# Performance work log

Measured on AMD Instinct MI355X. Metric: run time of the kernel, lower is better.

The kernel has to match this reference:

```python
import jax, jax.numpy as jnp
import numpy as np

D_MODEL = 1024
D_INNER = 2048        # expand=2
D_STATE = 128
NHEADS = 16           # d_inner / headdim
HEADDIM = 128
D_CONV = 4
D_XBC = D_INNER + 2 * D_STATE          # 2304 (ngroups=1)
D_IN_PROJ = 2 * D_INNER + 2 * D_STATE + NHEADS  # 4368
BATCH, SEQLEN = 2, 2048
EPS = 1e-5


def setup_inputs() -> dict:
    key = jax.random.key(0)
    ks = jax.random.split(key, 8)
    f = jnp.float32
    return {
        "x": jax.random.normal(ks[0], (BATCH, SEQLEN, D_MODEL), f),
        "ln_w": jnp.ones((D_MODEL,), f),
        "ln_b": jnp.zeros((D_MODEL,), f),
        "W_in": jax.random.normal(ks[1], (D_MODEL, D_IN_PROJ), f) * 0.02,
        "conv_w": jax.random.normal(ks[2], (D_XBC, D_CONV), f) * 0.2,
        "conv_b": jnp.zeros((D_XBC,), f),
        "dt_bias": jax.random.uniform(ks[3], (NHEADS,), f, -4.0, -2.0),
        "A_log": jnp.log(jax.random.uniform(ks[4], (NHEADS,), f, 1.0, 16.0)),
        "D": jnp.ones((NHEADS,), f),
        "rms_w": jnp.ones((D_INNER,), f),
        "W_out": jax.random.normal(ks[5], (D_INNER, D_MODEL), f) * 0.02,
    }


def _mamba_wrap(x, ln_w, ln_b, W_in, conv_w, conv_b, dt_bias, A_log, D, rms_w, W_out):
    B, L = x.shape[0], x.shape[1]
    # LayerNorm (pre-norm)
    mu = jnp.mean(x, -1, keepdims=True)
    var = jnp.mean(jnp.square(x - mu), -1, keepdims=True)
    xn = (x - mu) * jax.lax.rsqrt(var + EPS) * ln_w + ln_b
    # input projection -> z, xBC, dt
    zxbcdt = xn @ W_in                               # (B,L,4368)
    z = zxbcdt[..., :D_INNER]                        # (B,L,2048)
    xBC = zxbcdt[..., D_INNER:D_INNER + D_XBC]       # (B,L,2304)
    dt = jax.nn.softplus(zxbcdt[..., -NHEADS:] + dt_bias)  # (B,L,16)
    # causal depthwise conv1d (kernel 4), then SiLU
    xp = jnp.pad(xBC, ((0, 0), (D_CONV - 1, 0), (0, 0)))
    taps = jnp.stack([xp[:, k:k + L, :] for k in range(D_CONV)], axis=-1)  # (B,L,C,K)
    xBC = jax.nn.silu(jnp.einsum('blck,ck->blc', taps, conv_w) + conv_b)
    # split into SSM inputs
    xh = xBC[..., :D_INNER].reshape(B, L, NHEADS, HEADDIM)   # (B,L,H,P)
    Bm = xBC[..., D_INNER:D_INNER + D_STATE]                  # (B,L,N) ngroups=1
    Cm = xBC[..., D_INNER + D_STATE:]                         # (B,L,N)
    A = -jnp.exp(A_log)                                       # (H,)
    dA = jnp.exp(dt * A)                                      # (B,L,H)

    def step(state, inp):
        xt, dtt, dAt, Bt, Ct = inp  # (B,H,P),(B,H),(B,H),(B,N),(B,N)
        state = state * dAt[..., None, None] + (dtt[..., None] * xt)[..., None] * Bt[:, None, None, :]
        y = jnp.einsum('bhpn,bn->bhp', state, Ct)
        return state, y

    init = jnp.zeros((B, NHEADS, HEADDIM, D_STATE), x.dtype)
    xs = (xh.transpose(1, 0, 2, 3), dt.transpose(1, 0, 2), dA.transpose(1, 0, 2),
          Bm.transpose(1, 0, 2), Cm.transpose(1, 0, 2))
    _, ys = jax.lax.scan(step, init, xs)                      # (L,B,H,P)
    y = ys.transpose(1, 0, 2, 3) + D[None, None, :, None] * xh  # skip term
    y = y.reshape(B, L, D_INNER)
    # gated RMSNorm: rmsnorm(y * silu(z)) * weight
    y = y * jax.nn.silu(z)
    y = y * jax.lax.rsqrt(jnp.mean(y * y, -1, keepdims=True) + EPS) * rms_w
    # output projection + residual
    return x + y @ W_out


def reference(x, ln_w, ln_b, W_in, conv_w, conv_b, dt_bias, A_log, D, rms_w, W_out):
    return _mamba_wrap(x, ln_w, ln_b, W_in, conv_w, conv_b, dt_bias, A_log, D, rms_w, W_out)
```

## Files before the change

kernel.cpp:

```cpp
#include <hip/hip_runtime.h>

typedef unsigned short ushort_t;
typedef __attribute__((ext_vector_type(8))) unsigned short ushort8;
typedef __attribute__((ext_vector_type(4))) unsigned short ushortv4;
typedef __attribute__((ext_vector_type(8))) __bf16 bf16x8;
typedef __attribute__((ext_vector_type(4))) float f32x4;

#define BATCH   2
#define SEQLEN  2048
#define BL      4096
#define DMODEL  1024
#define DINNER  2048
#define DSTATE  128
#define NHEADS  16
#define DXBC    2304
#define DPROJ   4368
#define NPAD    4480
#define EPSF    1e-5f
#define QCH     128
#define NCH     16
#define BH      32

#define SWZ(row, colbyte) ((colbyte) ^ (((row) & 7) << 4))

#define GLDS(gp, lp) __builtin_amdgcn_global_load_lds( \
    (const __attribute__((address_space(1))) void*)(gp), \
    (__attribute__((address_space(3))) void*)(lp), 16, 0, 0)

__device__ __forceinline__ float bf2f(ushort_t h) {
    unsigned int u = ((unsigned int)h) << 16;
    float f; __builtin_memcpy(&f, &u, 4); return f;
}
__device__ __forceinline__ ushort_t f2bf(float f) {
    unsigned int u; __builtin_memcpy(&u, &f, 4);
    unsigned int r = u + 0x7fffu + ((u >> 16) & 1u);
    return (ushort_t)(r >> 16);
}
__device__ __forceinline__ float siluf(float x) { return x / (1.f + expf(-x)); }
__device__ __forceinline__ float softplusf(float x) { return (x > 20.f) ? x : log1pf(expf(x)); }

__global__ __launch_bounds__(256) void ln_kernel(const float* __restrict__ x,
        const float* __restrict__ w, const float* __restrict__ b, ushort_t* __restrict__ xn) {
    int r = blockIdx.x, t = threadIdx.x;
    const float* xr = x + (size_t)r * DMODEL;
    float4 v = *(const float4*)&xr[t * 4];
    float s  = v.x + v.y + v.z + v.w;
    float sq = v.x*v.x + v.y*v.y + v.z*v.z + v.w*v.w;
    __shared__ float red[8];
    #pragma unroll
    for (int m = 32; m >= 1; m >>= 1) { s += __shfl_xor(s, m, 64); sq += __shfl_xor(sq, m, 64); }
    int wv = t >> 6;
    if ((t & 63) == 0) { red[wv] = s; red[4 + wv] = sq; }
    __syncthreads();
    s  = red[0] + red[1] + red[2] + red[3];
    sq = red[4] + red[5] + red[6] + red[7];
    float mu  = s * (1.f / DMODEL);
    float var = sq * (1.f / DMODEL) - mu * mu;
    float inv = rsqrtf(var + EPSF);
    float4 wv4 = *(const float4*)&w[t * 4];
    float4 bv4 = *(const float4*)&b[t * 4];
    ushortv4 o;
    o[0] = f2bf((v.x - mu) * inv * wv4.x + bv4.x);
    o[1] = f2bf((v.y - mu) * inv * wv4.y + bv4.y);
    o[2] = f2bf((v.z - mu) * inv * wv4.z + bv4.z);
    o[3] = f2bf((v.w - mu) * inv * wv4.w + bv4.w);
    *(ushortv4*)&xn[(size_t)r * DMODEL + t * 4] = o;
}

__global__ __launch_bounds__(256) void transpose_cast(const float* __restrict__ W,
        ushort_t* __restrict__ WT, int K, int N) {
    __shared__ float tile[32][33];
    int n0 = blockIdx.x * 32, k0 = blockIdx.y * 32;
    int tx = threadIdx.x & 31, ty = threadIdx.x >> 5;
    #pragma unroll
    for (int i = 0; i < 32; i += 8) {
        int n = n0 + tx;
        tile[ty + i][tx] = (n < N) ? W[(size_t)(k0 + ty + i) * N + n] : 0.f;
    }
    __syncthreads();
    #pragma unroll
    for (int i = 0; i < 32; i += 8) {
        WT[(size_t)(n0 + ty + i) * K + k0 + tx] = f2bf(tile[tx][ty + i]);
    }
}

__global__ __launch_bounds__(256) void convw_tr(const float* __restrict__ w,
        float* __restrict__ wt) {
    int c = blockIdx.x * 256 + threadIdx.x;
    if (c < DXBC) {
        float4 v = *(const float4*)&w[c * 4];
        wt[0 * DXBC + c] = v.x;
        wt[1 * DXBC + c] = v.y;
        wt[2 * DXBC + c] = v.z;
        wt[3 * DXBC + c] = v.w;
    }
}

template <bool OUTBF>
__global__ __launch_bounds__(256) void gemm_bt(const ushort_t* __restrict__ A,
        const ushort_t* __restrict__ BT, void* __restrict__ Cv,
        const float* __restrict__ resid, int K, int ldc, int nbx) {
    const int tid = threadIdx.x;
    const int nwg = gridDim.x;
    const int cpx = nwg >> 3;
    const int lid = (blockIdx.x & 7) * cpx + (blockIdx.x >> 3);
    const int m0 = (lid / nbx) * 128, n0 = (lid % nbx) * 128;
    __shared__ ushort_t As[3][128 * 32];
    __shared__ ushort_t Bs[3][128 * 32];
    const int lane = tid & 63, wave = tid >> 6;
    const int wrow = wave * 32;
    const int srow = lane >> 2;
    const int selm = ((lane & 3) ^ (srow & 3)) * 8;
    const ushort_t* ag0 = A  + (size_t)(m0 + wrow + srow) * K + selm;
    const ushort_t* ag1 = ag0 + (size_t)16 * K;
    const ushort_t* bg0 = BT + (size_t)(n0 + wrow + srow) * K + selm;
    const ushort_t* bg1 = bg0 + (size_t)16 * K;
    const int wm = (wave >> 1) * 64, wn = (wave & 1) * 64;
    const int fr = lane & 15, ko = (lane >> 4) * 8;
    f32x4 acc[4][4];
    #pragma unroll
    for (int i = 0; i < 4; i++)
        #pragma unroll
        for (int j = 0; j < 4; j++) acc[i][j] = (f32x4){0.f, 0.f, 0.f, 0.f};
    const int nt = K >> 5;
    #pragma unroll
    for (int t = 0; t < 3; t++) {
        const size_t kof = (size_t)t * 32;
        GLDS(ag0 + kof, &As[t][wrow * 32]);
        GLDS(ag1 + kof, &As[t][(wrow + 16) * 32]);
        GLDS(bg0 + kof, &Bs[t][wrow * 32]);
        GLDS(bg1 + kof, &Bs[t][(wrow + 16) * 32]);
    }
    asm volatile("s_waitcnt vmcnt(8)" ::: "memory");
    __builtin_amdgcn_s_barrier();
    int cur = 0;
    for (int t = 0; t < nt; ++t) {
        if (t + 2 < nt) {
            int nb = cur + 2; if (nb >= 3) nb -= 3;
            const size_t kof = (size_t)(t + 2) * 32;
            GLDS(ag0 + kof, &As[nb][wrow * 32]);
            GLDS(ag1 + kof, &As[nb][(wrow + 16) * 32]);
            GLDS(bg0 + kof, &Bs[nb][wrow * 32]);
            GLDS(bg1 + kof, &Bs[nb][(wrow + 16) * 32]);
        }
        bf16x8 af[4], bfr[4];
        #pragma unroll
        for (int i = 0; i < 4; i++) {
            int row = wm + i * 16 + fr;
            af[i] = *(const bf16x8*)((const char*)&As[cur][0] + row * 64
                                     + ((ko * 2) ^ ((row & 3) << 4)));
        }
        #pragma unroll
        for (int j = 0; j < 4; j++) {
            int row = wn + j * 16 + fr;
            bfr[j] = *(const bf16x8*)((const char*)&Bs[cur][0] + row * 64
                                      + ((ko * 2) ^ ((row & 3) << 4)));
        }
        #pragma unroll
        for (int i = 0; i < 4; i++)
            #pragma unroll
            for (int j = 0; j < 4; j++)
                acc[i][j] = __builtin_amdgcn_mfma_f32_16x16x32_bf16(af[i], bfr[j], acc[i][j], 0, 0, 0);
        if (t + 2 < nt) asm volatile("s_waitcnt vmcnt(4)" ::: "memory");
        else            asm volatile("s_waitcnt vmcnt(0)" ::: "memory");
        __builtin_amdgcn_s_barrier();
        cur = (cur == 2) ? 0 : cur + 1;
    }
    const int r0 = (lane >> 4) * 4;
    #pragma unroll
    for (int i = 0; i < 4; i++)
        #pragma unroll
        for (int j = 0; j < 4; j++)
            #pragma unroll
            for (int r = 0; r < 4; r++) {
                int m = m0 + wm + i * 16 + r0 + r;
                int n = n0 + wn + j * 16 + fr;
                float v = acc[i][j][r];
                if (OUTBF) {
                    ((ushort_t*)Cv)[(size_t)m * ldc + n] = f2bf(v);
                } else {
                    if (resid) v += resid[(size_t)m * ldc + n];
                    ((float*)Cv)[(size_t)m * ldc + n] = v;
                }
            }
}

__global__ __launch_bounds__(256) void conv_kernel(const ushort_t* __restrict__ zxb,
        const float* __restrict__ wtr, const float* __restrict__ conv_b,
        const float* __restrict__ dt_bias, const float* __restrict__ A_log,
        ushort_t* __restrict__ xcv, ushort_t* __restrict__ Bcg, ushort_t* __restrict__ Ccg,
        float* __restrict__ dtv, float* __restrict__ dta) {
    int bid = blockIdx.x;
    int l = bid & (SEQLEN - 1);
    int tid = threadIdx.x;
    const ushort_t* rowp = zxb + (size_t)bid * NPAD;
    #pragma unroll 1
    for (int u = tid; u < DXBC / 8; u += 256) {
        int c0 = u * 8;
        float acc[8];
        {
            float4 b0 = *(const float4*)&conv_b[c0];
            float4 b1 = *(const float4*)&conv_b[c0 + 4];
            acc[0] = b0.x; acc[1] = b0.y; acc[2] = b0.z; acc[3] = b0.w;
            acc[4] = b1.x; acc[5] = b1.y; acc[6] = b1.z; acc[7] = b1.w;
        }
        #pragma unroll
        for (int k = 0; k < 4; k++) {
            int ll = l - 3 + k;
            if (ll >= 0) {
                ushort8 xv = *(const ushort8*)&rowp[(ptrdiff_t)(k - 3) * NPAD + DINNER + c0];
                float4 w0 = *(const float4*)&wtr[k * DXBC + c0];
                float4 w1 = *(const float4*)&wtr[k * DXBC + c0 + 4];
                acc[0] += bf2f((ushort_t)xv[0]) * w0.x;
                acc[1] += bf2f((ushort_t)xv[1]) * w0.y;
                acc[2] += bf2f((ushort_t)xv[2]) * w0.z;
                acc[3] += bf2f((ushort_t)xv[3]) * w0.w;
                acc[4] += bf2f((ushort_t)xv[4]) * w1.x;
                acc[5] += bf2f((ushort_t)xv[5]) * w1.y;
                acc[6] += bf2f((ushort_t)xv[6]) * w1.z;
                acc[7] += bf2f((ushort_t)xv[7]) * w1.w;
            }
        }
        ushort8 o;
        #pragma unroll
        for (int e = 0; e < 8; e++) o[e] = f2bf(siluf(acc[e]));
        if (c0 < DINNER)                *(ushort8*)&xcv[(size_t)bid * DINNER + c0] = o;
        else if (c0 < DINNER + DSTATE)  *(ushort8*)&Bcg[(size_t)bid * DSTATE + (c0 - DINNER)] = o;
        else                            *(ushort8*)&Ccg[(size_t)bid * DSTATE + (c0 - DINNER - DSTATE)] = o;
    }
    if (tid < NHEADS) {
        float raw = bf2f(rowp[DINNER + DXBC + tid]) + dt_bias[tid];
        float dt = softplusf(raw);
        float A = -expf(A_log[tid]);
        dtv[(size_t)bid * NHEADS + tid] = dt;
        dta[(size_t)bid * NHEADS + tid] = dt * A;
    }
}

__global__ __launch_bounds__(128) void cumsum_kernel(const float* __restrict__ dta,
        const float* __restrict__ dtv, float* __restrict__ cabuf, float* __restrict__ expca,
        float* __restrict__ wbuf, float* __restrict__ dtbuf, float* __restrict__ dtot) {
    const int c = blockIdx.x, h = blockIdx.y, b = blockIdx.z;
    const int bh = b * NHEADS + h;
    const int j = threadIdx.x;
    const size_t row = (size_t)b * SEQLEN + c * QCH + j;
    float v  = dta[row * NHEADS + h];
    float dt = dtv[row * NHEADS + h];
    float pv = v;
    #pragma unroll
    for (int off = 1; off < 64; off <<= 1) {
        float u = __shfl_up(pv, off, 64);
        if ((j & 63) >= off) pv += u;
    }
    __shared__ float wsum[2];
    if ((j & 63) == 63) wsum[j >> 6] = pv;
    __syncthreads();
    float tot = wsum[0] + wsum[1];
    if (j >= 64) pv += wsum[0];
    const size_t idx = ((size_t)bh * NCH + c) * QCH + j;
    cabuf[idx] = pv;
    expca[idx] = expf(pv);
    wbuf[idx]  = expf(tot - pv) * dt;
    dtbuf[idx] = dt;
    if (j == 0) dtot[bh * NCH + c] = expf(tot);
}

__global__ __launch_bounds__(256) void chunkstate_kernel(const ushort_t* __restrict__ xcv,
        const ushort_t* __restrict__ Bcg, const float* __restrict__ wbuf,
        ushort_t* __restrict__ states) {
    const int c = blockIdx.x, h = blockIdx.y, b = blockIdx.z;
    const int bh = b * NHEADS + h;
    const int tid = threadIdx.x;
    __shared__ ushort_t Xt[128 * 128];
    __shared__ ushort_t Bt[128 * 128];
    __shared__ float wsh[QCH];
    if (tid < QCH) wsh[tid] = wbuf[((size_t)bh * NCH + c) * QCH + tid];
    __syncthreads();
    const size_t row0 = (size_t)b * SEQLEN + c * QCH;
    {
        const int f = tid & 127;
        const int jh = (tid >> 7) * 64;
        const ushort_t* xsrc = xcv + (row0 + jh) * DINNER + h * 128 + f;
        const ushort_t* bsrc = Bcg + (row0 + jh) * DSTATE + f;
        char* xrow = (char*)Xt + f * 256;
        char* brow = (char*)Bt + f * 256;
        #pragma unroll 2
        for (int e8 = 0; e8 < 8; e8++) {
            ushort8 tx, tb;
            #pragma unroll
            for (int e = 0; e < 8; e++) {
                int j = e8 * 8 + e;
                tx[e] = xsrc[(size_t)j * DINNER];
                tb[e] = f2bf(bf2f(bsrc[(size_t)j * DSTATE]) * wsh[jh + j]);
            }
            int cb = (jh + e8 * 8) * 2;
            *(ushort8*)(xrow + SWZ(f, cb)) = tx;
            *(ushort8*)(brow + SWZ(f, cb)) = tb;
        }
    }
    __syncthreads();
    const int lane = tid & 63, wave = tid >> 6;
    const int wp = (wave >> 1) * 64, wn = (wave & 1) * 64;
    const int fr = lane & 15, ko = (lane >> 4) * 8;
    f32x4 acc[4][4];
    #pragma unroll
    for (int i = 0; i < 4; i++)
        #pragma unroll
        for (int j = 0; j < 4; j++) acc[i][j] = (f32x4){0.f, 0.f, 0.f, 0.f};
    for (int k0 = 0; k0 < 128; k0 += 32) {
        bf16x8 af[4], bfr[4];
        #pragma unroll
        for (int i = 0; i < 4; i++) {
            int rp = wp + i * 16 + fr;
            af[i] = *(const bf16x8*)((const char*)Xt + rp * 256 + SWZ(rp, (k0 + ko) * 2));
        }
        #pragma unroll
        for (int j = 0; j < 4; j++) {
            int rn = wn + j * 16 + fr;
            bfr[j] = *(const bf16x8*)((const char*)Bt + rn * 256 + SWZ(rn, (k0 + ko) * 2));
        }
        #pragma unroll
        for (int i = 0; i < 4; i++)
            #pragma unroll
            for (int j = 0; j < 4; j++)
                acc[i][j] = __builtin_amdgcn_mfma_f32_16x16x32_bf16(af[i], bfr[j], acc[i][j], 0, 0, 0);
    }
    const int r0 = (lane >> 4) * 4;
    ushort_t* outp = states + ((size_t)bh * NCH + c) * 16384;
    #pragma unroll
    for (int i = 0; i < 4; i++)
        #pragma unroll
        for (int j = 0; j < 4; j++)
            #pragma unroll
            for (int r = 0; r < 4; r++)
                outp[(wp + i * 16 + r0 + r) * 128 + wn + j * 16 + fr] = f2bf(acc[i][j][r]);
}

__global__ __launch_bounds__(256) void statescan_kernel(ushort_t* __restrict__ states,
        const float* __restrict__ dtot) {
    const int pseg = blockIdx.x, bh = blockIdx.y;
    const int tid = threadIdx.x;
    const int p = pseg * 8 + (tid >> 5);
    const int n4 = (tid & 31) * 4;
    ushort_t* base = states + (size_t)bh * NCH * 16384 + p * 128 + n4;
    const float* dtp = dtot + bh * NCH;
    float r0 = 0.f, r1 = 0.f, r2 = 0.f, r3 = 0.f;
    #pragma unroll 1
    for (int c = 0; c < NCH; c++) {
        ushortv4* ptr = (ushortv4*)(base + (size_t)c * 16384);
        ushortv4 cs = *ptr;
        ushortv4 o;
        o[0] = f2bf(r0); o[1] = f2bf(r1); o[2] = f2bf(r2); o[3] = f2bf(r3);
        *ptr = o;
        float d = dtp[c];
        r0 = r0 * d + bf2f(cs[0]);
        r1 = r1 * d + bf2f(cs[1]);
        r2 = r2 * d + bf2f(cs[2]);
        r3 = r3 * d + bf2f(cs[3]);
    }
}

__global__ __launch_bounds__(256) void chunkout_kernel(const ushort_t* __restrict__ xcv,
        const ushort_t* __restrict__ Bcg, const ushort_t* __restrict__ Ccg,
        const ushort_t* __restrict__ states, const float* __restrict__ cabuf,
        const float* __restrict__ expca, const float* __restrict__ dtbuf,
        const float* __restrict__ Dvec, ushort_t* __restrict__ yv) {
    const int c = blockIdx.x, h = blockIdx.y, b = blockIdx.z;
    const int bh = b * NHEADS + h;
    const int tid = threadIdx.x;
    __shared__ ushort_t R1[128 * 128];
    __shared__ ushort_t R2[128 * 128];
    __shared__ float cash[QCH], dtsh[QCH], exsh[QCH];
    const size_t aidx = ((size_t)bh * NCH + c) * QCH;
    if (tid < QCH) {
        cash[tid] = cabuf[aidx + tid];
        dtsh[tid] = dtbuf[aidx + tid];
        exsh[tid] = expca[aidx + tid];
    }
    const size_t row0 = (size_t)b * SEQLEN + c * QCH;
    {
        const ushort_t* sp = states + ((size_t)bh * NCH + c) * 16384;
        #pragma unroll
        for (int it = 0; it < 8; it++) {
            int g = tid + it * 256;
            int r = g >> 4, n8 = (g & 15) * 8;
            ushort8 vc = *(const ushort8*)&Ccg[(row0 + r) * DSTATE + n8];
            ushort8 vs = *(const ushort8*)&sp[r * 128 + n8];
            int cb = n8 * 2;
            *(ushort8*)((char*)R2 + r * 256 + SWZ(r, cb)) = vc;
            *(ushort8*)((char*)R1 + r * 256 + SWZ(r, cb)) = vs;
        }
    }
    __syncthreads();
    const int lane = tid & 63, wave = tid >> 6;
    const int fr = lane & 15, ko = (lane >> 4) * 8, r0 = (lane >> 4) * 4;
    const int wty = (wave >> 1) * 64, wpy = (wave & 1) * 64;
    f32x4 y_[4][4];
    #pragma unroll
    for (int i = 0; i < 4; i++)
        #pragma unroll
        for (int j = 0; j < 4; j++) y_[i][j] = (f32x4){0.f, 0.f, 0.f, 0.f};
    for (int k0 = 0; k0 < 128; k0 += 32) {
        bf16x8 af[4], bfr[4];
        #pragma unroll
        for (int i = 0; i < 4; i++) {
            int rt = wty + i * 16 + fr;
            af[i] = *(const bf16x8*)((const char*)R2 + rt * 256 + SWZ(rt, (k0 + ko) * 2));
        }
        #pragma unroll
        for (int j = 0; j < 4; j++) {
            int rp = wpy + j * 16 + fr;
            bfr[j] = *(const bf16x8*)((const char*)R1 + rp * 256 + SWZ(rp, (k0 + ko) * 2));
        }
        #pragma unroll
        for (int i = 0; i < 4; i++)
            #pragma unroll
            for (int j = 0; j < 4; j++)
                y_[i][j] = __builtin_amdgcn_mfma_f32_16x16x32_bf16(af[i], bfr[j], y_[i][j], 0, 0, 0);
    }
    #pragma unroll
    for (int i = 0; i < 4; i++)
        #pragma unroll
        for (int r = 0; r < 4; r++) {
            float sc = exsh[wty + i * 16 + r0 + r];
            #pragma unroll
            for (int j = 0; j < 4; j++) y_[i][j][r] *= sc;
        }
    __syncthreads();
    #pragma unroll
    for (int it = 0; it < 8; it++) {
        int g = tid + it * 256;
        int r = g >> 4, n8 = (g & 15) * 8;
        ushort8 vb = *(const ushort8*)&Bcg[(row0 + r) * DSTATE + n8];
        *(ushort8*)((char*)R1 + r * 256 + SWZ(r, n8 * 2)) = vb;
    }
    __syncthreads();
    const int wj = (wave >> 1) * 64, wt = (wave & 1) * 64;
    f32x4 g_[4][4];
    #pragma unroll
    for (int i = 0; i < 4; i++)
        #pragma unroll
        for (int t = 0; t < 4; t++) g_[i][t] = (f32x4){0.f, 0.f, 0.f, 0.f};
    if (!(wj == 64 && wt == 0)) {
        for (int k0 = 0; k0 < 128; k0 += 32) {
            bf16x8 af[4], bfr[4];
            #pragma unroll
            for (int i = 0; i < 4; i++) {
                int rj = wj + i * 16 + fr;
                af[i] = *(const bf16x8*)((const char*)R1 + rj * 256 + SWZ(rj, (k0 + ko) * 2));
            }
            #pragma unroll
            for (int t = 0; t < 4; t++) {
                int rt = wt + t * 16 + fr;
                bfr[t] = *(const bf16x8*)((const char*)R2 + rt * 256 + SWZ(rt, (k0 + ko) * 2));
            }
            #pragma unroll
            for (int i = 0; i < 4; i++)
                #pragma unroll
                for (int t = 0; t < 4; t++)
                    g_[i][t] = __builtin_amdgcn_mfma_f32_16x16x32_bf16(af[i], bfr[t], g_[i][t], 0, 0, 0);
        }
    }
    __syncthreads();
    {
        const float Dh = Dvec[h];
        #pragma unroll
        for (int i = 0; i < 4; i++) {
            #pragma unroll
            for (int t = 0; t < 4; t++) {
                int tt = wt + t * 16 + fr;
                int jj0 = wj + i * 16 + r0;
                ushortv4 pk;
                #pragma unroll
                for (int r = 0; r < 4; r++) {
                    int jj = jj0 + r;
                    float val = 0.f;
                    if (jj <= tt) {
                        val = g_[i][t][r] * expf(cash[tt] - cash[jj]) * dtsh[jj];
                        if (jj == tt) val += Dh;
                    }
                    pk[r] = f2bf(val);
                }
                *(ushortv4*)((char*)R1 + tt * 256 + SWZ(tt, jj0 * 2)) = pk;
            }
        }
        const int f = tid & 127;
        const int jh = (tid >> 7) * 64;
        const ushort_t* xsrc = xcv + (row0 + jh) * DINNER + h * 128 + f;
        char* xrow = (char*)R2 + f * 256;
        #pragma unroll 2
        for (int e8 = 0; e8 < 8; e8++) {
            ushort8 tx;
            #pragma unroll
            for (int e = 0; e < 8; e++) tx[e] = xsrc[(size_t)(e8 * 8 + e) * DINNER];
            int cb = (jh + e8 * 8) * 2;
            *(ushort8*)(xrow + SWZ(f, cb)) = tx;
        }
    }
    __syncthreads();
    const int kmax = wty + 64;
    for (int k0 = 0; k0 < kmax; k0 += 32) {
        bf16x8 af[4], bfr[4];
        #pragma unroll
        for (int i = 0; i < 4; i++) {
            int rt = wty + i * 16 + fr;
            af[i] = *(const bf16x8*)((const char*)R1 + rt * 256 + SWZ(rt, (k0 + ko) * 2));
        }
        #pragma unroll
        for (int j = 0; j < 4; j++) {
            int rp = wpy + j * 16 + fr;
            bfr[j] = *(const bf16x8*)((const char*)R2 + rp * 256 + SWZ(rp, (k0 + ko) * 2));
        }
        #pragma unroll
        for (int i = 0; i < 4; i++)
            #pragma unroll
            for (int j = 0; j < 4; j++)
                y_[i][j] = __builtin_amdgcn_mfma_f32_16x16x32_bf16(af[i], bfr[j], y_[i][j], 0, 0, 0);
    }
    #pragma unroll
    for (int i = 0; i < 4; i++)
        #pragma unroll
        for (int j = 0; j < 4; j++)
            #pragma unroll
            for (int r = 0; r < 4; r++) {
                int t = wty + i * 16 + r0 + r;
                int p = wpy + j * 16 + fr;
                yv[(row0 + t) * DINNER + h * 128 + p] = f2bf(y_[i][j][r]);
            }
}

__global__ __launch_bounds__(256) void gate_rms(const ushort_t* __restrict__ yv,
        const ushort_t* __restrict__ zxb, const float* __restrict__ rms_w,
        ushort_t* __restrict__ ynorm) {
    int r = blockIdx.x, t = threadIdx.x;
    const ushort_t* yr = yv + (size_t)r * DINNER;
    const ushort_t* zr = zxb + (size_t)r * NPAD;
    ushort8 y8 = *(const ushort8*)&yr[t * 8];
    ushort8 z8 = *(const ushort8*)&zr[t * 8];
    float g[8];
    #pragma unroll
    for (int j = 0; j < 8; j++)
        g[j] = bf2f((ushort_t)y8[j]) * siluf(bf2f((ushort_t)z8[j]));
    float sq = 0.f;
    #pragma unroll
    for (int j = 0; j < 8; j++) sq += g[j] * g[j];
    __shared__ float red[4];
    #pragma unroll
    for (int m = 32; m >= 1; m >>= 1) sq += __shfl_xor(sq, m, 64);
    int wv = t >> 6;
    if ((t & 63) == 0) red[wv] = sq;
    __syncthreads();
    sq = red[0] + red[1] + red[2] + red[3];
    float scale = rsqrtf(sq * (1.f / DINNER) + EPSF);
    float4 w0 = *(const float4*)&rms_w[t * 8];
    float4 w1 = *(const float4*)&rms_w[t * 8 + 4];
    ushort8 o;
    o[0] = f2bf(g[0] * scale * w0.x);
    o[1] = f2bf(g[1] * scale * w0.y);
    o[2] = f2bf(g[2] * scale * w0.z);
    o[3] = f2bf(g[3] * scale * w0.w);
    o[4] = f2bf(g[4] * scale * w1.x);
    o[5] = f2bf(g[5] * scale * w1.y);
    o[6] = f2bf(g[6] * scale * w1.z);
    o[7] = f2bf(g[7] * scale * w1.w);
    *(ushort8*)&ynorm[(size_t)r * DINNER + t * 8] = o;
}

extern "C" void kernel_launch(void* const* d_in, const int* in_sizes, int n_in,
                              void* d_out, int out_size, void* d_ws, size_t ws_size,
                              hipStream_t stream) {
    (void)in_sizes; (void)n_in; (void)out_size; (void)ws_size;
    const float* x       = (const float*)d_in[0];
    const float* ln_w    = (const float*)d_in[1];
    const float* ln_b    = (const float*)d_in[2];
    const float* W_in    = (const float*)d_in[3];
    const float* conv_w  = (const float*)d_in[4];
    const float* conv_b  = (const float*)d_in[5];
    const float* dt_bias = (const float*)d_in[6];
    const float* A_log   = (const float*)d_in[7];
    const float* Dvec    = (const float*)d_in[8];
    const float* rms_w   = (const float*)d_in[9];
    const float* W_out   = (const float*)d_in[10];
    float* out = (float*)d_out;

    char* ws = (char*)d_ws;
    size_t off = 0;
    auto alloc = [&](size_t bytes) -> void* {
        void* p = ws + off;
        off += (bytes + 255) & ~(size_t)255;
        return p;
    };
    ushort_t* xn    = (ushort_t*)alloc((size_t)BL * DMODEL * 2);
    ushort_t* WinT  = (ushort_t*)alloc((size_t)NPAD * DMODEL * 2);
    ushort_t* zxb   = (ushort_t*)alloc((size_t)BL * NPAD * 2);
    ushort_t* xcv   = (ushort_t*)alloc((size_t)BL * DINNER * 2);
    ushort_t* Bcg   = (ushort_t*)alloc((size_t)BL * DSTATE * 2);
    ushort_t* Ccg   = (ushort_t*)alloc((size_t)BL * DSTATE * 2);
    float*    dtv   = (float*)   alloc((size_t)BL * NHEADS * 4);
    float*    dta   = (float*)   alloc((size_t)BL * NHEADS * 4);
    ushort_t* yv    = (ushort_t*)alloc((size_t)BL * DINNER * 2);
    ushort_t* ynorm = (ushort_t*)alloc((size_t)BL * DINNER * 2);
    ushort_t* WoutT = (ushort_t*)alloc((size_t)DMODEL * DINNER * 2);
    float*    wtr   = (float*)   alloc((size_t)4 * DXBC * 4);
    float*    cabuf = (float*)   alloc((size_t)BH * NCH * QCH * 4);
    float*    expcb = (float*)   alloc((size_t)BH * NCH * QCH * 4);
    float*    wbuf  = (float*)   alloc((size_t)BH * NCH * QCH * 4);
    float*    dtbuf = (float*)   alloc((size_t)BH * NCH * QCH * 4);
    float*    dtot  = (float*)   alloc((size_t)BH * NCH * 4);
    ushort_t* states= (ushort_t*)alloc((size_t)BH * NCH * 16384 * 2);

    ln_kernel<<<BL, 256, 0, stream>>>(x, ln_w, ln_b, xn);
    transpose_cast<<<dim3(NPAD / 32, DMODEL / 32), 256, 0, stream>>>(W_in, WinT, DMODEL, DPROJ);
    transpose_cast<<<dim3(DMODEL / 32, DINNER / 32), 256, 0, stream>>>(W_out, WoutT, DINNER, DMODEL);
    convw_tr<<<(DXBC + 255) / 256, 256, 0, stream>>>(conv_w, wtr);
    gemm_bt<true><<<(NPAD / 128) * (BL / 128), 256, 0, stream>>>(xn, WinT, zxb, nullptr, DMODEL, NPAD, NPAD / 128);
    conv_kernel<<<BL, 256, 0, stream>>>(zxb, wtr, conv_b, dt_bias, A_log, xcv, Bcg, Ccg, dtv, dta);
    cumsum_kernel<<<dim3(NCH, NHEADS, BATCH), 128, 0, stream>>>(dta, dtv, cabuf, expcb, wbuf, dtbuf, dtot);
    chunkstate_kernel<<<dim3(NCH, NHEADS, BATCH), 256, 0, stream>>>(xcv, Bcg, wbuf, states);
    statescan_kernel<<<dim3(16, BH), 256, 0, stream>>>(states, dtot);
    chunkout_kernel<<<dim3(NCH, NHEADS, BATCH), 256, 0, stream>>>(xcv, Bcg, Ccg, states, cabuf, expcb, dtbuf, Dvec, yv);
    gate_rms<<<BL, 256, 0, stream>>>(yv, zxb, rms_w, ynorm);
    gemm_bt<false><<<(DMODEL / 128) * (BL / 128), 256, 0, stream>>>(ynorm, WoutT, out, x, DINNER, DMODEL, DMODEL / 128);
}
```

Baseline: 208.3 us.

## Add 256x256-tile double-buffered GEMM for input projection

Introduces a new 512-thread GEMM kernel with 256x256 output tiles and 64-wide K steps, double-buffered through LDS with direct global-to-LDS loads, and uses it for the input projection. The projection width is padded to 4608 so it divides evenly into 256-column tiles. The larger tiles raise arithmetic intensity and cut redundant operand loads, but they use a lot of LDS and registers, which lowers occupancy. The grid also shrinks to 288 workgroups, which may balance poorly across the compute units. The padding adds extra wasted columns of compute.

```diff
diff --git a/kernel.cpp b/kernel.cpp
--- a/kernel.cpp
+++ b/kernel.cpp
@@ -15,7 +15,7 @@
 #define NHEADS  16
 #define DXBC    2304
 #define DPROJ   4368
-#define NPAD    4480
+#define NPAD    4608
 #define EPSF    1e-5f
 #define QCH     128
 #define NCH     16
@@ -96,9 +96,82 @@
     }
 }
 
-template <bool OUTBF>
+__global__ __launch_bounds__(512) void gemm256_bt(const ushort_t* __restrict__ A,
+        const ushort_t* __restrict__ BT, ushort_t* __restrict__ C,
+        int K, int ldc, int nbx) {
+    const int tid = threadIdx.x;
+    const int nwg = gridDim.x;
+    const int cpx = nwg >> 3;
+    const int lid = (blockIdx.x & 7) * cpx + (blockIdx.x >> 3);
+    const int m0 = (lid / nbx) * 256, n0 = (lid % nbx) * 256;
+    __shared__ ushort_t As[2][256 * 64];
+    __shared__ ushort_t Bs[2][256 * 64];
+    const int lane = tid & 63, wid = tid >> 6;
+    const int l8 = lane >> 3, c8 = lane & 7;
+    const int selm = (c8 ^ l8) * 8;
+    const ushort_t* aB = A  + (size_t)(m0 + wid * 8 + l8) * K + selm;
+    const ushort_t* bB = BT + (size_t)(n0 + wid * 8 + l8) * K + selm;
+    const int wm2 = wid >> 2, wn4 = wid & 3;
+    const int fr = lane & 15, ko2 = (lane >> 4) * 16;
+    f32x4 acc[8][4];
+    #pragma unroll
+    for (int i = 0; i < 8; i++)
+        #pragma unroll
+        for (int j = 0; j < 4; j++) acc[i][j] = (f32x4){0.f, 0.f, 0.f, 0.f};
+    const int nt = K >> 6;
+    #define ST256(slot, kt) do { \
+        const size_t kof = (size_t)(kt) * 64; \
+        _Pragma("unroll") \
+        for (int q = 0; q < 4; q++) { \
+            GLDS(aB + (size_t)q * 64 * K + kof, &As[slot][(q * 64 + wid * 8) * 64]); \
+            GLDS(bB + (size_t)q * 64 * K + kof, &Bs[slot][(q * 64 + wid * 8) * 64]); \
+        } \
+    } while (0)
+    ST256(0, 0);
+    asm volatile("s_waitcnt vmcnt(0)" ::: "memory");
+    __builtin_amdgcn_s_barrier();
+    int cur = 0;
+    for (int t = 0; t < nt; ++t) {
+        if (t + 1 < nt) ST256(cur ^ 1, t + 1);
+        #pragma unroll
+        for (int kh = 0; kh < 2; kh++) {
+            bf16x8 bq[4];
+            #pragma unroll
+            for (int nj = 0; nj < 4; nj++) {
+                int rn = wn4 * 64 + nj * 16 + fr;
+                int kb = (kh * 64 + ko2) ^ ((rn & 7) << 4);
+                bq[nj] = *(const bf16x8*)((const char*)&Bs[cur][0] + rn * 128 + kb);
+            }
+            #pragma unroll
+            for (int mi = 0; mi < 8; mi++) {
+                int row = wm2 * 128 + mi * 16 + fr;
+                int kb = (kh * 64 + ko2) ^ ((row & 7) << 4);
+                bf16x8 a = *(const bf16x8*)((const char*)&As[cur][0] + row * 128 + kb);
+                #pragma unroll
+                for (int nj = 0; nj < 4; nj++)
+                    acc[mi][nj] = __builtin_amdgcn_mfma_f32_16x16x32_bf16(a, bq[nj], acc[mi][nj], 0, 0, 0);
+            }
+        }
+        asm volatile("s_waitcnt vmcnt(0)" ::: "memory");
+        __builtin_amdgcn_s_barrier();
+        cur ^= 1;
+    }
+    const int r0 = (lane >> 4) * 4;
+    #pragma unroll
+    for (int mi = 0; mi < 8; mi++)
+        #pragma unroll
+        for (int nj = 0; nj < 4; nj++)
+            #pragma unroll
+            for (int r = 0; r < 4; r++) {
+                int m = m0 + wm2 * 128 + mi * 16 + r0 + r;
+                int n = n0 + wn4 * 64 + nj * 16 + fr;
+                C[(size_t)m * ldc + n] = f2bf(acc[mi][nj][r]);
+            }
+    #undef ST256
+}
+
 __global__ __launch_bounds__(256) void gemm_bt(const ushort_t* __restrict__ A,
-        const ushort_t* __restrict__ BT, void* __restrict__ Cv,
+        const ushort_t* __restrict__ BT, float* __restrict__ C,
         const float* __restrict__ resid, int K, int ldc, int nbx) {
     const int tid = threadIdx.x;
     const int nwg = gridDim.x;
@@ -176,12 +249,8 @@
                 int m = m0 + wm + i * 16 + r0 + r;
                 int n = n0 + wn + j * 16 + fr;
                 float v = acc[i][j][r];
-                if (OUTBF) {
-                    ((ushort_t*)Cv)[(size_t)m * ldc + n] = f2bf(v);
-                } else {
-                    if (resid) v += resid[(size_t)m * ldc + n];
-                    ((float*)Cv)[(size_t)m * ldc + n] = v;
-                }
+                if (resid) v += resid[(size_t)m * ldc + n];
+                C[(size_t)m * ldc + n] = v;
             }
 }
 
@@ -613,12 +682,12 @@
     transpose_cast<<<dim3(NPAD / 32, DMODEL / 32), 256, 0, stream>>>(W_in, WinT, DMODEL, DPROJ);
     transpose_cast<<<dim3(DMODEL / 32, DINNER / 32), 256, 0, stream>>>(W_out, WoutT, DINNER, DMODEL);
     convw_tr<<<(DXBC + 255) / 256, 256, 0, stream>>>(conv_w, wtr);
-    gemm_bt<true><<<(NPAD / 128) * (BL / 128), 256, 0, stream>>>(xn, WinT, zxb, nullptr, DMODEL, NPAD, NPAD / 128);
+    gemm256_bt<<<(NPAD / 256) * (BL / 256), 512, 0, stream>>>(xn, WinT, zxb, DMODEL, NPAD, NPAD / 256);
     conv_kernel<<<BL, 256, 0, stream>>>(zxb, wtr, conv_b, dt_bias, A_log, xcv, Bcg, Ccg, dtv, dta);
     cumsum_kernel<<<dim3(NCH, NHEADS, BATCH), 128, 0, stream>>>(dta, dtv, cabuf, expcb, wbuf, dtbuf, dtot);
     chunkstate_kernel<<<dim3(NCH, NHEADS, BATCH), 256, 0, stream>>>(xcv, Bcg, wbuf, states);
     statescan_kernel<<<dim3(16, BH), 256, 0, stream>>>(states, dtot);
     chunkout_kernel<<<dim3(NCH, NHEADS, BATCH), 256, 0, stream>>>(xcv, Bcg, Ccg, states, cabuf, expcb, dtbuf, Dvec, yv);
     gate_rms<<<BL, 256, 0, stream>>>(yv, zxb, rms_w, ynorm);
-    gemm_bt<false><<<(DMODEL / 128) * (BL / 128), 256, 0, stream>>>(ynorm, WoutT, out, x, DINNER, DMODEL, DMODEL / 128);
-}
+    gemm_bt<<<(DMODEL / 128) * (BL / 128), 256, 0, stream>>>(ynorm, WoutT, out, x, DINNER, DMODEL, DMODEL / 128);
+}
```

Result: slower. 217.1 us (+4.2%).
